# Performance work log

Hardware: AMD Instinct MI355X
Metric: run time of the kernel (lower is better)

The kernel has to match this reference:

```python
import jax, jax.numpy as jnp
import numpy as np

P = 128  # fixed patch width (coord[3k] == 128 for all k)


def setup_inputs() -> dict:
    key = jax.random.key(0)
    B, C, H, W = 32, 3, 512, 512
    inputs = jax.random.normal(key, (B, C, H, W), dtype=jnp.float32)
    j = np.arange(B)
    # (i1, i2) offsets matching the coord list in init_kwargs
    starts = jnp.asarray(
        np.stack([(37 * j) % (H - P), (53 * j) % (W - P)], axis=1),
        dtype=jnp.int32,
    )
    return {"inputs": inputs, "starts": starts}


def reference(inputs, starts):
    # inputs: [B, C, H, W] float32; starts: [B, 2] int32 (i1, i2 per image)
    B, C, H, W = inputs.shape

    def crop_resize(img, st):
        # crop PxP patch, then bilinear-upsample back to (H, W)
        patch = jax.lax.dynamic_slice(img, (0, st[0], st[1]), (C, P, P))
        # half-pixel-center bilinear == torch bilinear align_corners=False
        # (antialias is a no-op when upsampling)
        return jax.image.resize(patch, (C, H, W), method="bilinear")

    return jax.vmap(crop_resize)(inputs, starts)  # [B, C, H, W]
```

## Files before the change

kernel.cpp:

```cpp
#include <hip/hip_runtime.h>


#define PP   128
#define HH   512
#define WW   512
#define CC   3

typedef float f32x4 __attribute__((ext_vector_type(4)));

__global__ __launch_bounds__(256) void crop_resize4x_blk_kernel(
    const float* __restrict__ in,
    const int*   __restrict__ starts,
    float*       __restrict__ out)
{
    const int t  = blockIdx.x * blockDim.x + threadIdx.x;
    const int qx = t & 127;
    const int qy = (t >> 7) & 127;
    const int bc = t >> 14;
    const int b  = bc / 3;

    const int s0 = starts[2 * b];
    const int s1 = starts[2 * b + 1];
    const float* patch = in + ((size_t)bc * HH + s0) * WW + s1;

    const int ya = max(qy - 1, 0);
    const int yc = min(qy + 1, PP - 1);
    const int xa = max(qx - 1, 0);
    const int xc = min(qx + 1, PP - 1);

    const float* rA = patch + (size_t)ya * WW;
    const float* rB = patch + (size_t)qy * WW;
    const float* rC = patch + (size_t)yc * WW;

    const float aA = rA[xa], aB = rA[qx], aC = rA[xc];
    const float bA = rB[xa], bB = rB[qx], bC = rB[xc];
    const float cA = rC[xa], cB = rC[qx], cC = rC[xc];

    float vA[4], vB[4], vC[4];
    vA[0] = 0.375f * aA + 0.625f * bA;
    vB[0] = 0.375f * aB + 0.625f * bB;
    vC[0] = 0.375f * aC + 0.625f * bC;
    vA[1] = 0.125f * aA + 0.875f * bA;
    vB[1] = 0.125f * aB + 0.875f * bB;
    vC[1] = 0.125f * aC + 0.875f * bC;
    vA[2] = 0.875f * bA + 0.125f * cA;
    vB[2] = 0.875f * bB + 0.125f * cB;
    vC[2] = 0.875f * bC + 0.125f * cC;
    vA[3] = 0.625f * bA + 0.375f * cA;
    vB[3] = 0.625f * bB + 0.375f * cB;
    vC[3] = 0.625f * bC + 0.375f * cC;

    float* orow = out + ((size_t)bc * HH + ((size_t)qy << 2)) * WW + ((size_t)qx << 2);

    #pragma unroll
    for (int ry = 0; ry < 4; ++ry) {
        f32x4 o;
        o.x = 0.375f * vA[ry] + 0.625f * vB[ry];
        o.y = 0.125f * vA[ry] + 0.875f * vB[ry];
        o.z = 0.875f * vB[ry] + 0.125f * vC[ry];
        o.w = 0.625f * vB[ry] + 0.375f * vC[ry];
        *reinterpret_cast<f32x4*>(orow + (size_t)ry * WW) = o;
    }
}

extern "C" void kernel_launch(void* const* d_in, const int* in_sizes, int n_in,
                              void* d_out, int out_size, void* d_ws, size_t ws_size,
                              hipStream_t stream) {
    const float* in     = (const float*)d_in[0];
    const int*   starts = (const int*)d_in[1];
    float*       out    = (float*)d_out;

    const int B = in_sizes[1] / 2;
    const int total_threads = B * CC * PP * PP;
    const int block = 256;
    const int grid = (total_threads + block - 1) / block;

    crop_resize4x_blk_kernel<<<grid, block, 0, stream>>>(in, starts, out);
}
```

Baseline: 24.17 us.

## Compute four patch rows per thread with shared row loads and nontemporal stores

```diff
diff --git a/kernel.cpp b/kernel.cpp
--- a/kernel.cpp
+++ b/kernel.cpp
@@ -8,58 +8,70 @@
 
 typedef float f32x4 __attribute__((ext_vector_type(4)));
 
-__global__ __launch_bounds__(256) void crop_resize4x_blk_kernel(
+__global__ __launch_bounds__(256) void crop_resize4x_tall_kernel(
     const float* __restrict__ in,
     const int*   __restrict__ starts,
     float*       __restrict__ out)
 {
-    const int t  = blockIdx.x * blockDim.x + threadIdx.x;
-    const int qx = t & 127;
-    const int qy = (t >> 7) & 127;
-    const int bc = t >> 14;
-    const int b  = bc / 3;
+    const int bc  = blockIdx.x >> 4;
+    const int b   = bc / 3;
+    const int t   = (blockIdx.x << 8) | threadIdx.x;
+    const int qx  = t & 127;
+    const int qys = (t >> 7) & 31;
 
     const int s0 = starts[2 * b];
     const int s1 = starts[2 * b + 1];
     const float* patch = in + ((size_t)bc * HH + s0) * WW + s1;
 
-    const int ya = max(qy - 1, 0);
-    const int yc = min(qy + 1, PP - 1);
     const int xa = max(qx - 1, 0);
+    const int xb = qx;
     const int xc = min(qx + 1, PP - 1);
+    const int qy0 = qys << 2;
 
-    const float* rA = patch + (size_t)ya * WW;
-    const float* rB = patch + (size_t)qy * WW;
-    const float* rC = patch + (size_t)yc * WW;
+    float r[6][3];
+    #pragma unroll
+    for (int j = 0; j < 6; ++j) {
+        int ry = qy0 - 1 + j;
+        ry = min(max(ry, 0), PP - 1);
+        const float* row = patch + (size_t)ry * WW;
+        r[j][0] = row[xa];
+        r[j][1] = row[xb];
+        r[j][2] = row[xc];
+    }
 
-    const float aA = rA[xa], aB = rA[qx], aC = rA[xc];
-    const float bA = rB[xa], bB = rB[qx], bC = rB[xc];
-    const float cA = rC[xa], cB = rC[qx], cC = rC[xc];
-
-    float vA[4], vB[4], vC[4];
-    vA[0] = 0.375f * aA + 0.625f * bA;
-    vB[0] = 0.375f * aB + 0.625f * bB;
-    vC[0] = 0.375f * aC + 0.625f * bC;
-    vA[1] = 0.125f * aA + 0.875f * bA;
-    vB[1] = 0.125f * aB + 0.875f * bB;
-    vC[1] = 0.125f * aC + 0.875f * bC;
-    vA[2] = 0.875f * bA + 0.125f * cA;
-    vB[2] = 0.875f * bB + 0.125f * cB;
-    vC[2] = 0.875f * bC + 0.125f * cC;
-    vA[3] = 0.625f * bA + 0.375f * cA;
-    vB[3] = 0.625f * bB + 0.375f * cB;
-    vC[3] = 0.625f * bC + 0.375f * cC;
-
-    float* orow = out + ((size_t)bc * HH + ((size_t)qy << 2)) * WW + ((size_t)qx << 2);
+    float* obase = out + ((size_t)bc * HH + ((size_t)qys << 4)) * WW
+                       + ((size_t)qx << 2);
 
     #pragma unroll
-    for (int ry = 0; ry < 4; ++ry) {
-        f32x4 o;
-        o.x = 0.375f * vA[ry] + 0.625f * vB[ry];
-        o.y = 0.125f * vA[ry] + 0.875f * vB[ry];
-        o.z = 0.875f * vB[ry] + 0.125f * vC[ry];
-        o.w = 0.625f * vB[ry] + 0.375f * vC[ry];
-        *reinterpret_cast<f32x4*>(orow + (size_t)ry * WW) = o;
+    for (int g = 0; g < 4; ++g) {
+        const float aA = r[g][0],     aB = r[g][1],     aC = r[g][2];
+        const float bA = r[g + 1][0], bB = r[g + 1][1], bC = r[g + 1][2];
+        const float cA = r[g + 2][0], cB = r[g + 2][1], cC = r[g + 2][2];
+
+        float vA[4], vB[4], vC[4];
+        vA[0] = 0.375f * aA + 0.625f * bA;
+        vB[0] = 0.375f * aB + 0.625f * bB;
+        vC[0] = 0.375f * aC + 0.625f * bC;
+        vA[1] = 0.125f * aA + 0.875f * bA;
+        vB[1] = 0.125f * aB + 0.875f * bB;
+        vC[1] = 0.125f * aC + 0.875f * bC;
+        vA[2] = 0.875f * bA + 0.125f * cA;
+        vB[2] = 0.875f * bB + 0.125f * cB;
+        vC[2] = 0.875f * bC + 0.125f * cC;
+        vA[3] = 0.625f * bA + 0.375f * cA;
+        vB[3] = 0.625f * bB + 0.375f * cB;
+        vC[3] = 0.625f * bC + 0.375f * cC;
+
+        #pragma unroll
+        for (int ry = 0; ry < 4; ++ry) {
+            f32x4 o;
+            o.x = 0.375f * vA[ry] + 0.625f * vB[ry];
+            o.y = 0.125f * vA[ry] + 0.875f * vB[ry];
+            o.z = 0.875f * vB[ry] + 0.125f * vC[ry];
+            o.w = 0.625f * vB[ry] + 0.375f * vC[ry];
+            __builtin_nontemporal_store(
+                o, reinterpret_cast<f32x4*>(obase + (size_t)(4 * g + ry) * WW));
+        }
     }
 }
 
@@ -71,9 +83,6 @@
     float*       out    = (float*)d_out;
 
     const int B = in_sizes[1] / 2;
-    const int total_threads = B * CC * PP * PP;
-    const int block = 256;
-    const int grid = (total_threads + block - 1) / block;
-
-    crop_resize4x_blk_kernel<<<grid, block, 0, stream>>>(in, starts, out);
+    const int grid = B * CC * 16;
+    crop_resize4x_tall_kernel<<<grid, 256, 0, stream>>>(in, starts, out);
 }
```

New measurement: 22.28 us. -7.8%, faster.
